# Optimization experiments

Hardware: AMD Instinct MI355X
Metric: run time of the kernel (lower is better)

## Reference

```python
import jax, jax.numpy as jnp
import numpy as np

H_IMG, W_IMG = 160, 160
C1, C2, HEADS, NHOPS = 128, 256, 8, 2
N_NODES = H_IMG * W_IMG


def build_edges(H, W):
    # 3x3 neighborhood (excl. self) + skip edges (i+2,j),(i,j+2); self loops added once
    node = (np.arange(H)[:, None] * W + np.arange(W)[None, :])
    offsets = [(di, dj) for di in (-1, 0, 1) for dj in (-1, 0, 1) if (di, dj) != (0, 0)] + [(2, 0), (0, 2)]
    srcs, dsts = [], []
    for di, dj in offsets:
        i0, i1 = max(0, -di), H - max(0, di)
        j0, j1 = max(0, -dj), W - max(0, dj)
        srcs.append(node[i0:i1, j0:j1].ravel())
        dsts.append(node[i0 + di:i1 + di, j0 + dj:j1 + dj].ravel())
    n = np.arange(H * W)
    srcs.append(n); dsts.append(n)
    return (np.concatenate(srcs).astype(np.int32), np.concatenate(dsts).astype(np.int32))


def setup_inputs() -> dict:
    key = jax.random.key(0)
    ks = jax.random.split(key, 16)
    s = 0.05
    src_np, dst_np = build_edges(H_IMG, W_IMG)
    d = C2 // HEADS
    return {
        "x": jax.random.normal(ks[0], (1, C1, H_IMG, W_IMG), jnp.float32),
        "w_id": jax.random.normal(ks[1], (C2, C1), jnp.float32) * s,
        "w_in": jax.random.normal(ks[2], (C2, C1), jnp.float32) * s,
        "w_gat": jax.random.normal(ks[3], (NHOPS, C2, C2), jnp.float32) * s,
        "a_src": jax.random.normal(ks[4], (NHOPS, HEADS, d), jnp.float32) * s,
        "a_dst": jax.random.normal(ks[5], (NHOPS, HEADS, d), jnp.float32) * s,
        "gat_bias": jax.random.normal(ks[6], (NHOPS, C2), jnp.float32) * s,
        "bn_gamma": jax.random.uniform(ks[7], (NHOPS, C2), jnp.float32, 0.5, 1.5),
        "bn_beta": jax.random.normal(ks[8], (NHOPS, C2), jnp.float32) * s,
        "bn_mean": jax.random.normal(ks[9], (NHOPS, C2), jnp.float32) * s,
        "bn_var": jax.random.uniform(ks[10], (NHOPS, C2), jnp.float32, 0.5, 1.5),
        "w_out": jax.random.normal(ks[11], (C2, C2), jnp.float32) * s,
        "se_w1": jax.random.normal(ks[12], (C2 // 4, C2), jnp.float32) * s,
        "se_b1": jax.random.normal(ks[13], (C2 // 4,), jnp.float32) * s,
        "se_w2": jax.random.normal(ks[14], (C2, C2 // 4), jnp.float32) * s,
        "se_b2": jax.random.normal(ks[15], (C2,), jnp.float32) * s,
        "src": jnp.asarray(src_np),
        "dst": jnp.asarray(dst_np),
    }


def _gat(x, W, a_s, a_d, b, src, dst, N):
    heads, d = a_s.shape
    h = (x @ W.T).reshape(N, heads, d)                      # [N,H,D]
    al_s = jnp.einsum('nhd,hd->nh', h, a_s)                 # [N,H]
    al_d = jnp.einsum('nhd,hd->nh', h, a_d)
    e = jax.nn.leaky_relu(al_s[src] + al_d[dst], 0.2)       # [E,H]
    emax = jax.lax.stop_gradient(jax.ops.segment_max(e, dst, num_segments=N))
    ee = jnp.exp(e - emax[dst])
    denom = jax.ops.segment_sum(ee, dst, num_segments=N)
    alpha = ee / (denom[dst] + 1e-16)                       # segment softmax over incoming edges
    out = jax.ops.segment_sum(h[src] * alpha[..., None], dst, num_segments=N)
    return out.reshape(N, heads * d) + b


def _forward(x, w_id, w_in, w_gat, a_src, a_dst, gat_bias, bn_gamma, bn_beta,
             bn_mean, bn_var, w_out, se_w1, se_b1, se_w2, se_b2, src, dst):
    identity = jnp.einsum('bchw,oc->bohw', x, w_id)
    h = jnp.einsum('bchw,oc->bohw', x, w_in)
    B, C, H, W = h.shape
    N = B * H * W
    xf = h.transpose(0, 2, 3, 1).reshape(N, C)
    for l in range(NHOPS):
        res = xf
        g = _gat(xf, w_gat[l], a_src[l], a_dst[l], gat_bias[l], src, dst, N)
        g = (g - bn_mean[l]) * (bn_gamma[l] * jax.lax.rsqrt(bn_var[l] + 1e-5)) + bn_beta[l]
        xf = jax.nn.relu(g) + res
    y = xf.reshape(B, H, W, C).transpose(0, 3, 1, 2)
    y = jnp.einsum('bchw,oc->bohw', y, w_out)
    # SE block
    w = y.mean(axis=(2, 3))                                 # [B,C]
    w = jax.nn.relu(w @ se_w1.T + se_b1)
    w = jax.nn.sigmoid(w @ se_w2.T + se_b2)
    y = y * w[:, :, None, None]
    return y + identity


def reference(x, w_id, w_in, w_gat, a_src, a_dst, gat_bias, bn_gamma, bn_beta,
              bn_mean, bn_var, w_out, se_w1, se_b1, se_w2, se_b2, src, dst):
    return _forward(x, w_id, w_in, w_gat, a_src, a_dst, gat_bias, bn_gamma, bn_beta,
                    bn_mean, bn_var, w_out, se_w1, se_b1, se_w2, se_b2, src, dst)
```

## Files before the change

kernel.cpp:

```cpp
#include <hip/hip_runtime.h>

#define NN 25600
#define HH 160
#define WW 160
#define C2 256

#define B_WIN   0
#define B_WID   32768
#define B_WGAT  65536
#define B_WOUT  196608
#define B_WEND  262144

#define C_BNA   0
#define C_BNB   512
#define C_ASRC  1024
#define C_ADST  1536
#define C_SEW1  2048
#define C_SEB1  18432
#define C_SEW2  18496
#define C_SEB2  34880
#define C_END   35136

typedef __attribute__((ext_vector_type(8))) short bfrag;
typedef __attribute__((ext_vector_type(4))) float ffrag;
// ... 36 lines not shown
    unsigned short* __restrict__ wb, float* __restrict__ cvt,
    float* __restrict__ means, unsigned short* __restrict__ xT)
{
    __shared__ unsigned short T[64 * 136];
    const bool f32 = probe_f32(xp);
    const int tid = threadIdx.x;
    const int bid = blockIdx.x;
    const int gid = bid * 256 + tid;
    const int stride = gridDim.x * 256;

    if (bid == 0) means[tid] = 0.f;

    for (int i = gid; i < B_WEND; i += stride) {
        const void* s; int o;
        if      (i < B_WID)   { s = pwin;  o = i - B_WIN; }
        else if (i < B_WGAT)  { s = pwid;  o = i - B_WID; }
        else if (i < B_WOUT)  { s = pwgat; o = i - B_WGAT; }
        else                  { s = pwout; o = i - B_WOUT; }
        wb[i] = f32 ? f2b(((const float*)s)[o]) : ((const unsigned short*)s)[o];
    }
    for (int i = gid; i < 512; i += stride) {
        float sc = ldf(pbng, i, f32) * rsqrtf(ldf(pbnv, i, f32) + 1e-5f);
        cvt[C_BNA + i] = sc;
        cvt[C_BNB + i] = (ldf(pgbias, i, f32) - ldf(pbnm, i, f32)) * sc + ldf(pbnb, i, f32);
        cvt[C_ASRC + i] = ldf(pasrc, i, f32);
        cvt[C_ADST + i] = ldf(padst, i, f32);
    }
    for (int i = gid; i < 16384; i += stride) {
        cvt[C_SEW1 + i] = ldf(psew1, i, f32);
        cvt[C_SEW2 + i] = ldf(psew2, i, f32);
    }
    for (int i = gid; i < 64; i += stride)  cvt[C_SEB1 + i] = ldf(pseb1, i, f32);
    for (int i = gid; i < 256; i += stride) cvt[C_SEB2 + i] = ldf(pseb2, i, f32);

    {
        const int n0 = bid * 64;
        const int nl = tid & 63;
#pragma unroll
        for (int i = 0; i < 32; ++i) {
            int c = i * 4 + (tid >> 6);
            long idx = (long)c * NN + n0 + nl;
            T[nl * 136 + c] = f32 ? f2b(((const float*)xp)[idx]) : xp[idx];
        }
        __syncthreads();
#pragma unroll
        for (int i = 0; i < 4; ++i) {
            int n = tid >> 2, c0 = (tid & 3) * 32 + i * 8;
            uint4 v = *(const uint4*)&T[n * 136 + c0];
            *(uint4*)(xT + (long)(n0 + n) * 128 + c0) = v;
        }
    }
}

struct SmemG2 { unsigned short As[128*40], Bi[64*40], Bd[64*40]; };
struct SmemG  { unsigned short As[128*40], Bs[64*40]; };
struct SmemC  { unsigned short Cs[128*72]; };
union  SmemX2 { SmemG2 s; SmemC c; };
union  SmemNN { SmemG s; SmemC c; };

__global__ __launch_bounds__(256) void mfma_gemm_x2_kernel(
    const unsigned short* __restrict__ A16,
    const unsigned short* __restrict__ Wi16,
    const unsigned short* __restrict__ Wd16,
    unsigned short* __restrict__ xf16,
    unsigned short* __restrict__ idb16)
{
    __shared__ SmemX2 sm;
    const int tid = threadIdx.x;
    const int m0 = blockIdx.x * 128, o0 = blockIdx.y * 64;
    const int lane = tid & 63, wv = tid >> 6;
    const int wm = wv >> 1, wn = wv & 1;
    const int lr = lane & 15, quad = lane >> 4;

    ffrag ai[4][2], ad[4][2];
#pragma unroll
    for (int mt = 0; mt < 4; ++mt)
#pragma unroll
        for (int nt = 0; nt < 2; ++nt) { ai[mt][nt] = (ffrag){0,0,0,0}; ad[mt][nt] = (ffrag){0,0,0,0}; }

    for (int k0 = 0; k0 < 128; k0 += 32) {
#pragma unroll
        for (int c = tid; c < 512; c += 256) {
            int row = c >> 2, q = c & 3;
            uint4 v = *(const uint4*)(A16 + (long)(m0 + row) * 128 + k0 + q * 8);
            *(uint4*)&sm.s.As[row * 40 + q * 8] = v;
        }
        {
            int row = tid >> 2, q = tid & 3;
            uint4 vi = *(const uint4*)(Wi16 + (long)(o0 + row) * 128 + k0 + q * 8);
            uint4 vd = *(const uint4*)(Wd16 + (long)(o0 + row) * 128 + k0 + q * 8);
            *(uint4*)&sm.s.Bi[row * 40 + q * 8] = vi;
            *(uint4*)&sm.s.Bd[row * 40 + q * 8] = vd;
        }
        __syncthreads();
        bfrag a[4], bi[2], bd[2];
#pragma unroll
        for (int mt = 0; mt < 4; ++mt)
            a[mt] = *(const bfrag*)&sm.s.As[(wm * 64 + mt * 16 + lr) * 40 + quad * 8];
#pragma unroll
        for (int nt = 0; nt < 2; ++nt) {
            bi[nt] = *(const bfrag*)&sm.s.Bi[(wn * 32 + nt * 16 + lr) * 40 + quad * 8];
            bd[nt] = *(const bfrag*)&sm.s.Bd[(wn * 32 + nt * 16 + lr) * 40 + quad * 8];
        }
#pragma unroll
        for (int mt = 0; mt < 4; ++mt)
#pragma unroll
            for (int nt = 0; nt < 2; ++nt) {
                ai[mt][nt] = __builtin_amdgcn_mfma_f32_16x16x32_bf16(a[mt], bi[nt], ai[mt][nt], 0, 0, 0);
                ad[mt][nt] = __builtin_amdgcn_mfma_f32_16x16x32_bf16(a[mt], bd[nt], ad[mt][nt], 0, 0, 0);
            }
        __syncthreads();
    }
#pragma unroll
    for (int mt = 0; mt < 4; ++mt)
#pragma unroll
        for (int nt = 0; nt < 2; ++nt)
#pragma unroll
            for (int r = 0; r < 4; ++r)
                sm.c.Cs[(wm * 64 + mt * 16 + quad * 4 + r) * 72 + wn * 32 + nt * 16 + lr] = f2b(ai[mt][nt][r]);
    __syncthreads();
#pragma unroll
    for (int it = 0; it < 4; ++it) {
        int e = it * 256 + tid;
        int row = e >> 3, c8 = (e & 7) * 8;
        *(uint4*)(xf16 + (long)(m0 + row) * C2 + o0 + c8) = *(const uint4*)&sm.c.Cs[row * 72 + c8];
    }
    __syncthreads();
#pragma unroll
    for (int mt = 0; mt < 4; ++mt)
#pragma unroll
        for (int nt = 0; nt < 2; ++nt)
#pragma unroll
            for (int r = 0; r < 4; ++r)
                sm.c.Cs[(wm * 64 + mt * 16 + quad * 4 + r) * 72 + wn * 32 + nt * 16 + lr] = f2b(ad[mt][nt][r]);
    __syncthreads();
#pragma unroll
    for (int it = 0; it < 4; ++it) {
        int e = it * 256 + tid;
        int row = e >> 3, c8 = (e & 7) * 8;
        *(uint4*)(idb16 + (long)(m0 + row) * C2 + o0 + c8) = *(const uint4*)&sm.c.Cs[row * 72 + c8];
    }
}

__global__ __launch_bounds__(256) void mfma_gemm_nn_kernel(
    const unsigned short* __restrict__ A16,
    const unsigned short* __restrict__ W16,
    unsigned short* __restrict__ C16,
    const float* __restrict__ asrc, const float* __restrict__ adst,
    float* __restrict__ al_s, float* __restrict__ al_d,
    float* __restrict__ means,
    int mode)
{
    __shared__ SmemNN sm;
    const int tid = threadIdx.x;
    const int m0 = blockIdx.x * 128, o0 = blockIdx.y * 64;
    const int lane = tid & 63, wv = tid >> 6;
    const int wm = wv >> 1, wn = wv & 1;
    const int lr = lane & 15, quad = lane >> 4;

    ffrag acc[4][2];
#pragma unroll
    for (int mt = 0; mt < 4; ++mt)
#pragma unroll
        for (int nt = 0; nt < 2; ++nt) acc[mt][nt] = (ffrag){0,0,0,0};

    for (int k0 = 0; k0 < 256; k0 += 32) {
#pragma unroll
        for (int c = tid; c < 512; c += 256) {
            int row = c >> 2, q = c & 3;
            uint4 v = *(const uint4*)(A16 + (long)(m0 + row) * 256 + k0 + q * 8);
            *(uint4*)&sm.s.As[row * 40 + q * 8] = v;
        }
        {
            int row = tid >> 2, q = tid & 3;
            uint4 v = *(const uint4*)(W16 + (long)(o0 + row) * 256 + k0 + q * 8);
            *(uint4*)&sm.s.Bs[row * 40 + q * 8] = v;
        }
        __syncthreads();
        bfrag a[4], b[2];
#pragma unroll
        for (int mt = 0; mt < 4; ++mt)
            a[mt] = *(const bfrag*)&sm.s.As[(wm * 64 + mt * 16 + lr) * 40 + quad * 8];
#pragma unroll
        for (int nt = 0; nt < 2; ++nt)
            b[nt] = *(const bfrag*)&sm.s.Bs[(wn * 32 + nt * 16 + lr) * 40 + quad * 8];
#pragma unroll
        for (int mt = 0; mt < 4; ++mt)
#pragma unroll
            for (int nt = 0; nt < 2; ++nt)
                acc[mt][nt] = __builtin_amdgcn_mfma_f32_16x16x32_bf16(a[mt], b[nt], acc[mt][nt], 0, 0, 0);
        __syncthreads();
    }
#pragma unroll
    for (int mt = 0; mt < 4; ++mt)
#pragma unroll
        for (int nt = 0; nt < 2; ++nt)
#pragma unroll
            for (int r = 0; r < 4; ++r)
                sm.c.Cs[(wm * 64 + mt * 16 + quad * 4 + r) * 72 + wn * 32 + nt * 16 + lr] = f2b(acc[mt][nt][r]);
    __syncthreads();
#pragma unroll
    for (int it = 0; it < 4; ++it) {
        int e = it * 256 + tid;
        int row = e >> 3, c8 = (e & 7) * 8;
        *(uint4*)(C16 + (long)(m0 + row) * C2 + o0 + c8) = *(const uint4*)&sm.c.Cs[row * 72 + c8];
    }
    if (mode == 1) {
        const int head = blockIdx.y * 2 + wn;
        const float as0 = asrc[head * 32 + lr], as1 = asrc[head * 32 + 16 + lr];
        const float ad0 = adst[head * 32 + lr], ad1 = adst[head * 32 + 16 + lr];
#pragma unroll
        for (int mt = 0; mt < 4; ++mt)
#pragma unroll
            for (int r = 0; r < 4; ++r) {
                float ps = acc[mt][0][r] * as0 + acc[mt][1][r] * as1;
                float pd = acc[mt][0][r] * ad0 + acc[mt][1][r] * ad1;
#pragma unroll
                for (int sh = 1; sh < 16; sh <<= 1) {
                    ps += __shfl_xor(ps, sh);
                    pd += __shfl_xor(pd, sh);
                }
                if (lr == 0) {
                    int m = m0 + wm * 64 + mt * 16 + quad * 4 + r;
                    al_s[m * 8 + head] = ps;
                    al_d[m * 8 + head] = pd;
                }
            }
    } else if (mode == 2) {
#pragma unroll
        for (int nt = 0; nt < 2; ++nt) {
            float p = 0.f;
#pragma unroll
            for (int mt = 0; mt < 4; ++mt)
#pragma unroll
                for (int r = 0; r < 4; ++r) p += acc[mt][nt][r];
            p += __shfl_xor(p, 16);
            p += __shfl_xor(p, 32);
            if (quad == 0) atomicAdd(&means[o0 + wn * 32 + nt * 16 + lr], p);
        }
    }
}

__global__ __launch_bounds__(256) void aggregate_kernel(
    const unsigned short* __restrict__ h16,
    const float* __restrict__ al_s,
    const float* __restrict__ al_d,
    const float* __restrict__ bnA,
    const float* __restrict__ bnB,
    unsigned short* __restrict__ xf16)
{
    const int SI[11] = { 1, 1, 1, 0, 0, -1, -1, -1, -2,  0, 0};
    const int SJ[11] = { 1, 0,-1, 1,-1,  1,  0, -1,  0, -2, 0};
    __shared__ float es[8][11][8];
    __shared__ float alpha[8][11][8];

    const int t = threadIdx.x;
    const int ln = t >> 5;
    const int l = t & 31;
    const int n = blockIdx.x * 8 + ln;
    const int i = n / WW, j = n % WW;

    for (int idx = t; idx < 704; idx += 256) {
        int lln = idx / 88, rem = idx - lln * 88;
        int k = rem >> 3, hh = rem & 7;
        int nn2 = blockIdx.x * 8 + lln;
        int ii = nn2 / WW, jj = nn2 - ii * WW;
        int si = ii + SI[k], sj = jj + SJ[k];
        bool okk = (si >= 0) & (si < HH) & (sj >= 0) & (sj < WW);
        es[lln][k][hh] = okk ? al_s[(si * WW + sj) * 8 + hh] : -1e30f;
    }
    __syncthreads();

    if (l < 8) {
        const int hd = l;
        const float ald = al_d[n * 8 + hd];
        float e[11];
        float mx = -1e30f;
#pragma unroll
        for (int k = 0; k < 11; ++k) {
            float v = es[ln][k][hd] + ald;
            v = v > 0.f ? v : 0.2f * v;
            e[k] = v;
            mx = fmaxf(mx, v);
        }
        float denom = 0.f;
#pragma unroll
        for (int k = 0; k < 11; ++k) {
            float p = __expf(e[k] - mx);
            e[k] = p;
            denom += p;
        }
        const float inv = 1.f / (denom + 1e-16f);
#pragma unroll
        for (int k = 0; k < 11; ++k) alpha[ln][k][hd] = e[k] * inv;
    }
    __syncthreads();

    const int c8 = l * 8;
    const int hd = l >> 2;
    int srcn[11];
#pragma unroll
    for (int k = 0; k < 11; ++k) {
        int si = i + SI[k], sj = j + SJ[k];
        bool ok = (si >= 0) & (si < HH) & (sj >= 0) & (sj < WW);
        srcn[k] = ok ? si * WW + sj : n;
    }
    float a0=0.f,a1=0.f,a2=0.f,a3=0.f,a4=0.f,a5=0.f,a6=0.f,a7=0.f;
#pragma unroll
    for (int k = 0; k < 11; ++k) {
        float al = alpha[ln][k][hd];
        uint4 hv = *(const uint4*)(h16 + (long)srcn[k] * C2 + c8);
        a0 += al * lo16f(hv.x); a1 += al * hi16f(hv.x);
        a2 += al * lo16f(hv.y); a3 += al * hi16f(hv.y);
        a4 += al * lo16f(hv.z); a5 += al * hi16f(hv.z);
        a6 += al * lo16f(hv.w); a7 += al * hi16f(hv.w);
    }
    float acc8[8] = {a0,a1,a2,a3,a4,a5,a6,a7};
    uint4 rv = *(const uint4*)(xf16 + (long)n * C2 + c8);
    float res[8] = {lo16f(rv.x),hi16f(rv.x),lo16f(rv.y),hi16f(rv.y),
                    lo16f(rv.z),hi16f(rv.z),lo16f(rv.w),hi16f(rv.w)};
    float out[8];
#pragma unroll
    for (int q = 0; q < 8; ++q) {
        int c = c8 + q;
        float g = acc8[q] * bnA[c] + bnB[c];
        out[q] = fmaxf(g, 0.f) + res[q];
    }
    ushort4 o16a, o16b;
    o16a.x = f2b(out[0]); o16a.y = f2b(out[1]); o16a.z = f2b(out[2]); o16a.w = f2b(out[3]);
    o16b.x = f2b(out[4]); o16b.y = f2b(out[5]); o16b.z = f2b(out[6]); o16b.w = f2b(out[7]);
    *(ushort4*)(xf16 + (long)n * C2 + c8)     = o16a;
    *(ushort4*)(xf16 + (long)n * C2 + c8 + 4) = o16b;
}

__global__ __launch_bounds__(256) void final_kernel(
    const unsigned short* __restrict__ x_probe,
    const unsigned short* __restrict__ y16,
    const unsigned short* __restrict__ idb16,
    const float* __restrict__ means,
    const float* __restrict__ cvt,
    void* __restrict__ outp)
{
    __shared__ float T[64][65];
    __shared__ float mv[256];
    __shared__ float hv[64];
    __shared__ float sv[64];
    const bool f32o = probe_f32(x_probe);
    const int t = threadIdx.x;
    const int n0 = blockIdx.x * 64, c0 = blockIdx.y * 64;

    mv[t] = means[t] * (1.0f / 25600.0f);
    __syncthreads();
    if (t < 64) {
        const float* w1 = cvt + C_SEW1 + t * 256;
        float s = cvt[C_SEB1 + t];
        for (int cc = 0; cc < 256; cc += 4) {
            float4 wv = *(const float4*)(w1 + cc);
            s += wv.x * mv[cc] + wv.y * mv[cc+1] + wv.z * mv[cc+2] + wv.w * mv[cc+3];
        }
        hv[t] = fmaxf(s, 0.f);
    }
    __syncthreads();
    if (t < 64) {
        const int c = c0 + t;
        const float* w2 = cvt + C_SEW2 + c * 64;
        float s = cvt[C_SEB2 + c];
        for (int k = 0; k < 64; k += 4) {
            float4 wv = *(const float4*)(w2 + k);
            s += wv.x * hv[k] + wv.y * hv[k+1] + wv.z * hv[k+2] + wv.w * hv[k+3];
        }
        sv[t] = 1.0f / (1.0f + __expf(-s));
    }
    __syncthreads();
#pragma unroll
    for (int it = 0; it < 16; ++it) {
        int e = t + it * 256;
        int nn = e >> 6, cc = e & 63;
        long idx = (long)(n0 + nn) * C2 + c0 + cc;
        T[cc][nn] = b2f(y16[idx]) * sv[cc] + b2f(idb16[idx]);
    }
    __syncthreads();
#pragma unroll
    for (int it = 0; it < 16; ++it) {
        int e = t + it * 256;
        int cc = e >> 6, nn = e & 63;
        long idx = (long)(c0 + cc) * NN + n0 + nn;
        float v = T[cc][nn];
        if (f32o) ((float*)outp)[idx] = v;
        else      ((unsigned short*)outp)[idx] = f2b(v);
    }
}

extern "C" void kernel_launch(void* const* d_in, const int* in_sizes, int n_in,
                              void* d_out, int out_size, void* d_ws, size_t ws_size,
                              hipStream_t stream) {
    float* ws = (float*)d_ws;
    float* cvt   = ws;
    float* means = ws + 35200;
    float* als   = means + 256;
    float* ald   = als + 204800;
    unsigned short* wb16  = (unsigned short*)(ald + 204800);
    unsigned short* xT16  = wb16 + B_WEND;
    unsigned short* xf16  = xT16 + NN * 128;
    unsigned short* h16   = xf16 + NN * 256;
    unsigned short* idb16 = h16 + NN * 256;

    const unsigned short* xp = (const unsigned short*)d_in[0];

    dim3 b256(256);
    dim3 gmfma(NN / 128, C2 / 64);
    dim3 gfin(NN / 64, C2 / 64);

    prep_kernel<<<400, b256, 0, stream>>>(
        xp, d_in[2], d_in[1], d_in[3], d_in[11],
        d_in[4], d_in[5], d_in[6], d_in[7], d_in[8], d_in[9], d_in[10],
        d_in[12], d_in[13], d_in[14], d_in[15],
        wb16, cvt, means, xT16);

    mfma_gemm_x2_kernel<<<gmfma, b256, 0, stream>>>(
        xT16, wb16 + B_WIN, wb16 + B_WID, xf16, idb16);

    for (int l = 0; l < 2; ++l) {
        mfma_gemm_nn_kernel<<<gmfma, b256, 0, stream>>>(
            xf16, wb16 + B_WGAT + l * 65536, h16,
            cvt + C_ASRC + l * 256, cvt + C_ADST + l * 256, als, ald, nullptr, 1);
        aggregate_kernel<<<NN / 8, b256, 0, stream>>>(h16, als, ald,
            cvt + C_BNA + l * 256, cvt + C_BNB + l * 256, xf16);
    }

    mfma_gemm_nn_kernel<<<gmfma, b256, 0, stream>>>(
        xf16, wb16 + B_WOUT, h16, nullptr, nullptr, nullptr, nullptr, means, 2);
    final_kernel<<<gfin, b256, 0, stream>>>(xp, h16, idb16, means, cvt, d_out);
}
```

Before: 239.7 us.

## Fuse GAT aggregation into following GEMM with full-width 512-thread tiles

Result: slower. 294.1 us (+22.7%).

```diff
diff --git a/kernel.cpp b/kernel.cpp
--- a/kernel.cpp
+++ b/kernel.cpp
@@ -113,10 +113,12 @@
 }
 
 struct SmemG2 { unsigned short As[128*40], Bi[64*40], Bd[64*40]; };
-struct SmemG  { unsigned short As[128*40], Bs[64*40]; };
 struct SmemC  { unsigned short Cs[128*72]; };
 union  SmemX2 { SmemG2 s; SmemC c; };
-union  SmemNN { SmemG s; SmemC c; };
+
+struct SmemFG { unsigned short As[128*40], Bs[256*40]; };
+struct SmemFA { float es[128][11][8]; };
+union  SmemF  { SmemFG g; SmemFA a; SmemC c; };
 
 __global__ __launch_bounds__(256) void mfma_gemm_x2_kernel(
     const unsigned short* __restrict__ A16,
@@ -202,93 +204,157 @@
     }
 }
 
-__global__ __launch_bounds__(256) void mfma_gemm_nn_kernel(
-    const unsigned short* __restrict__ A16,
+__global__ __launch_bounds__(512) void fused_gat_kernel(
+    unsigned short* __restrict__ xf16,
+    const unsigned short* __restrict__ h_in,
+    const float* __restrict__ als_in, const float* __restrict__ ald_in,
+    const float* __restrict__ bnA, const float* __restrict__ bnB,
     const unsigned short* __restrict__ W16,
-    unsigned short* __restrict__ C16,
+    unsigned short* __restrict__ Cout,
     const float* __restrict__ asrc, const float* __restrict__ adst,
-    float* __restrict__ al_s, float* __restrict__ al_d,
-    float* __restrict__ means,
-    int mode)
+    float* __restrict__ als_out, float* __restrict__ ald_out,
+    float* __restrict__ means, int mode)
 {
-    __shared__ SmemNN sm;
+    __shared__ SmemF sm;
     const int tid = threadIdx.x;
-    const int m0 = blockIdx.x * 128, o0 = blockIdx.y * 64;
+    const int m0 = blockIdx.x * 128;
     const int lane = tid & 63, wv = tid >> 6;
-    const int wm = wv >> 1, wn = wv & 1;
+    const int wm = wv >> 2, wn = wv & 3;
     const int lr = lane & 15, quad = lane >> 4;
 
-    ffrag acc[4][2];
+    const int SI[11] = { 1, 1, 1, 0, 0, -1, -1, -1, -2,  0, 0};
+    const int SJ[11] = { 1, 0,-1, 1,-1,  1,  0, -1,  0, -2, 0};
+
+    if (h_in) {
+        for (int idx = tid; idx < 11264; idx += 512) {
+            int ln = idx / 88, rem = idx - ln * 88;
+            int k = rem >> 3, hh = rem & 7;
+            int n2 = m0 + ln, ii = n2 / WW, jj = n2 - ii * WW;
+            int si = ii + SI[k], sj = jj + SJ[k];
+            bool ok = (si >= 0) & (si < HH) & (sj >= 0) & (sj < WW);
+            sm.a.es[ln][k][hh] = ok ? als_in[(si * WW + sj) * 8 + hh] : -1e30f;
+        }
+        __syncthreads();
+        for (int p = tid; p < 1024; p += 512) {
+            int ln = p >> 3, hd = p & 7;
+            float ad = ald_in[(m0 + ln) * 8 + hd];
+            float e[11];
+            float mx = -1e30f;
+#pragma unroll
+            for (int k = 0; k < 11; ++k) {
+                float v = sm.a.es[ln][k][hd] + ad;
+                v = v > 0.f ? v : 0.2f * v;
+                e[k] = v;
+                mx = fmaxf(mx, v);
+            }
+            float den = 0.f;
+#pragma unroll
+            for (int k = 0; k < 11; ++k) { float q = __expf(e[k] - mx); e[k] = q; den += q; }
+            float inv = 1.f / (den + 1e-16f);
+#pragma unroll
+            for (int k = 0; k < 11; ++k) sm.a.es[ln][k][hd] = e[k] * inv;
+        }
+        __syncthreads();
+        {
+            const int cj = tid & 31, c8 = cj * 8, hd = cj >> 2;
+            for (int q = 0; q < 8; ++q) {
+                int ln = q * 16 + (tid >> 5);
+                int n = m0 + ln, i = n / WW, j = n - i * WW;
+                float acc8[8] = {0,0,0,0,0,0,0,0};
+#pragma unroll
+                for (int k = 0; k < 11; ++k) {
+                    int si = i + SI[k], sj = j + SJ[k];
+                    bool ok = (si >= 0) & (si < HH) & (sj >= 0) & (sj < WW);
+                    int srcn = ok ? si * WW + sj : n;
+                    float al = sm.a.es[ln][k][hd];
+                    uint4 hv = *(const uint4*)(h_in + (long)srcn * C2 + c8);
+                    acc8[0] += al * lo16f(hv.x); acc8[1] += al * hi16f(hv.x);
+                    acc8[2] += al * lo16f(hv.y); acc8[3] += al * hi16f(hv.y);
+                    acc8[4] += al * lo16f(hv.z); acc8[5] += al * hi16f(hv.z);
+                    acc8[6] += al * lo16f(hv.w); acc8[7] += al * hi16f(hv.w);
+                }
+                uint4 rv = *(const uint4*)(xf16 + (long)n * C2 + c8);
+                float res[8] = {lo16f(rv.x),hi16f(rv.x),lo16f(rv.y),hi16f(rv.y),
+                                lo16f(rv.z),hi16f(rv.z),lo16f(rv.w),hi16f(rv.w)};
+                unsigned short o[8];
+#pragma unroll
+                for (int q2 = 0; q2 < 8; ++q2) {
+                    int c = c8 + q2;
+                    float g = acc8[q2] * bnA[c] + bnB[c];
+                    o[q2] = f2b(fmaxf(g, 0.f) + res[q2]);
+                }
+                uint4 ov;
+                ov.x = (unsigned int)o[0] | ((unsigned int)o[1] << 16);
+                ov.y = (unsigned int)o[2] | ((unsigned int)o[3] << 16);
+                ov.z = (unsigned int)o[4] | ((unsigned int)o[5] << 16);
+                ov.w = (unsigned int)o[6] | ((unsigned int)o[7] << 16);
+                *(uint4*)(xf16 + (long)n * C2 + c8) = ov;
+            }
+        }
+        __syncthreads();
+    }
+
+    ffrag acc[4][4];
 #pragma unroll
     for (int mt = 0; mt < 4; ++mt)
 #pragma unroll
-        for (int nt = 0; nt < 2; ++nt) acc[mt][nt] = (ffrag){0,0,0,0};
+        for (int nt = 0; nt < 4; ++nt) acc[mt][nt] = (ffrag){0,0,0,0};
 
     for (int k0 = 0; k0 < 256; k0 += 32) {
-#pragma unroll
-        for (int c = tid; c < 512; c += 256) {
-            int row = c >> 2, q = c & 3;
-            uint4 v = *(const uint4*)(A16 + (long)(m0 + row) * 256 + k0 + q * 8);
-            *(uint4*)&sm.s.As[row * 40 + q * 8] = v;
-        }
         {
             int row = tid >> 2, q = tid & 3;
-            uint4 v = *(const uint4*)(W16 + (long)(o0 + row) * 256 + k0 + q * 8);
-            *(uint4*)&sm.s.Bs[row * 40 + q * 8] = v;
-        }
-        __syncthreads();
-        bfrag a[4], b[2];
+            uint4 v = *(const uint4*)(xf16 + (long)(m0 + row) * C2 + k0 + q * 8);
+            *(uint4*)&sm.g.As[row * 40 + q * 8] = v;
+        }
+#pragma unroll
+        for (int c = tid; c < 1024; c += 512) {
+            int row = c >> 2, q = c & 3;
+            uint4 v = *(const uint4*)(W16 + (long)row * C2 + k0 + q * 8);
+            *(uint4*)&sm.g.Bs[row * 40 + q * 8] = v;
+        }
+        __syncthreads();
+        bfrag a[4], b[4];
 #pragma unroll
         for (int mt = 0; mt < 4; ++mt)
-            a[mt] = *(const bfrag*)&sm.s.As[(wm * 64 + mt * 16 + lr) * 40 + quad * 8];
-#pragma unroll
-        for (int nt = 0; nt < 2; ++nt)
-            b[nt] = *(const bfrag*)&sm.s.Bs[(wn * 32 + nt * 16 + lr) * 40 + quad * 8];
+            a[mt] = *(const bfrag*)&sm.g.As[(wm * 64 + mt * 16 + lr) * 40 + quad * 8];
+#pragma unroll
+        for (int nt = 0; nt < 4; ++nt)
+            b[nt] = *(const bfrag*)&sm.g.Bs[(wn * 64 + nt * 16 + lr) * 40 + quad * 8];
 #pragma unroll
         for (int mt = 0; mt < 4; ++mt)
 #pragma unroll
-            for (int nt = 0; nt < 2; ++nt)
+            for (int nt = 0; nt < 4; ++nt)
                 acc[mt][nt] = __builtin_amdgcn_mfma_f32_16x16x32_bf16(a[mt], b[nt], acc[mt][nt], 0, 0, 0);
         __syncthreads();
     }
-#pragma unroll
-    for (int mt = 0; mt < 4; ++mt)
-#pragma unroll
-        for (int nt = 0; nt < 2; ++nt)
-#pragma unroll
-            for (int r = 0; r < 4; ++r)
-                sm.c.Cs[(wm * 64 + mt * 16 + quad * 4 + r) * 72 + wn * 32 + nt * 16 + lr] = f2b(acc[mt][nt][r]);
-    __syncthreads();
-#pragma unroll
-    for (int it = 0; it < 4; ++it) {
-        int e = it * 256 + tid;
-        int row = e >> 3, c8 = (e & 7) * 8;
-        *(uint4*)(C16 + (long)(m0 + row) * C2 + o0 + c8) = *(const uint4*)&sm.c.Cs[row * 72 + c8];
-    }
+
     if (mode == 1) {
-        const int head = blockIdx.y * 2 + wn;
-        const float as0 = asrc[head * 32 + lr], as1 = asrc[head * 32 + 16 + lr];
-        const float ad0 = adst[head * 32 + lr], ad1 = adst[head * 32 + 16 + lr];
-#pragma unroll
-        for (int mt = 0; mt < 4; ++mt)
-#pragma unroll
-            for (int r = 0; r < 4; ++r) {
-                float ps = acc[mt][0][r] * as0 + acc[mt][1][r] * as1;
-                float pd = acc[mt][0][r] * ad0 + acc[mt][1][r] * ad1;
-#pragma unroll
-                for (int sh = 1; sh < 16; sh <<= 1) {
-                    ps += __shfl_xor(ps, sh);
-                    pd += __shfl_xor(pd, sh);
+#pragma unroll
+        for (int hh = 0; hh < 2; ++hh) {
+            const int head = wn * 2 + hh;
+            const float as_lo = asrc[head * 32 + lr], as_hi = asrc[head * 32 + 16 + lr];
+            const float ad_lo = adst[head * 32 + lr], ad_hi = adst[head * 32 + 16 + lr];
+#pragma unroll
+            for (int mt = 0; mt < 4; ++mt)
+#pragma unroll
+                for (int r = 0; r < 4; ++r) {
+                    float ps = acc[mt][2*hh][r] * as_lo + acc[mt][2*hh+1][r] * as_hi;
+                    float pd = acc[mt][2*hh][r] * ad_lo + acc[mt][2*hh+1][r] * ad_hi;
+#pragma unroll
+                    for (int sh = 1; sh < 16; sh <<= 1) {
+                        ps += __shfl_xor(ps, sh);
+                        pd += __shfl_xor(pd, sh);
+                    }
+                    if (lr == 0) {
+                        int m = m0 + wm * 64 + mt * 16 + quad * 4 + r;
+                        als_out[m * 8 + head] = ps;
+                        ald_out[m * 8 + head] = pd;
+                    }
                 }
-                if (lr == 0) {
-                    int m = m0 + wm * 64 + mt * 16 + quad * 4 + r;
-                    al_s[m * 8 + head] = ps;
-                    al_d[m * 8 + head] = pd;
-                }
-            }
+        }
     } else if (mode == 2) {
 #pragma unroll
-        for (int nt = 0; nt < 2; ++nt) {
+        for (int nt = 0; nt < 4; ++nt) {
             float p = 0.f;
 #pragma unroll
             for (int mt = 0; mt < 4; ++mt)
@@ -296,101 +362,30 @@
                 for (int r = 0; r < 4; ++r) p += acc[mt][nt][r];
             p += __shfl_xor(p, 16);
             p += __shfl_xor(p, 32);
-            if (quad == 0) atomicAdd(&means[o0 + wn * 32 + nt * 16 + lr], p);
-        }
-    }
-}
-
-__global__ __launch_bounds__(256) void aggregate_kernel(
-    const unsigned short* __restrict__ h16,
-    const float* __restrict__ al_s,
-    const float* __restrict__ al_d,
-    const float* __restrict__ bnA,
-    const float* __restrict__ bnB,
-    unsigned short* __restrict__ xf16)
-{
-    const int SI[11] = { 1, 1, 1, 0, 0, -1, -1, -1, -2,  0, 0};
-    const int SJ[11] = { 1, 0,-1, 1,-1,  1,  0, -1,  0, -2, 0};
-    __shared__ float es[8][11][8];
-    __shared__ float alpha[8][11][8];
-
-    const int t = threadIdx.x;
-    const int ln = t >> 5;
-    const int l = t & 31;
-    const int n = blockIdx.x * 8 + ln;
-    const int i = n / WW, j = n % WW;
-
-    for (int idx = t; idx < 704; idx += 256) {
-        int lln = idx / 88, rem = idx - lln * 88;
-        int k = rem >> 3, hh = rem & 7;
-        int nn2 = blockIdx.x * 8 + lln;
-        int ii = nn2 / WW, jj = nn2 - ii * WW;
-        int si = ii + SI[k], sj = jj + SJ[k];
-        bool okk = (si >= 0) & (si < HH) & (sj >= 0) & (sj < WW);
-        es[lln][k][hh] = okk ? al_s[(si * WW + sj) * 8 + hh] : -1e30f;
-    }
-    __syncthreads();
-
-    if (l < 8) {
-        const int hd = l;
-        const float ald = al_d[n * 8 + hd];
-        float e[11];
-        float mx = -1e30f;
-#pragma unroll
-        for (int k = 0; k < 11; ++k) {
-            float v = es[ln][k][hd] + ald;
-            v = v > 0.f ? v : 0.2f * v;
-            e[k] = v;
-            mx = fmaxf(mx, v);
-        }
-        float denom = 0.f;
-#pragma unroll
-        for (int k = 0; k < 11; ++k) {
-            float p = __expf(e[k] - mx);
-            e[k] = p;
-            denom += p;
-        }
-        const float inv = 1.f / (denom + 1e-16f);
-#pragma unroll
-        for (int k = 0; k < 11; ++k) alpha[ln][k][hd] = e[k] * inv;
-    }
-    __syncthreads();
-
-    const int c8 = l * 8;
-    const int hd = l >> 2;
-    int srcn[11];
-#pragma unroll
-    for (int k = 0; k < 11; ++k) {
-        int si = i + SI[k], sj = j + SJ[k];
-        bool ok = (si >= 0) & (si < HH) & (sj >= 0) & (sj < WW);
-        srcn[k] = ok ? si * WW + sj : n;
-    }
-    float a0=0.f,a1=0.f,a2=0.f,a3=0.f,a4=0.f,a5=0.f,a6=0.f,a7=0.f;
-#pragma unroll
-    for (int k = 0; k < 11; ++k) {
-        float al = alpha[ln][k][hd];
-        uint4 hv = *(const uint4*)(h16 + (long)srcn[k] * C2 + c8);
-        a0 += al * lo16f(hv.x); a1 += al * hi16f(hv.x);
-        a2 += al * lo16f(hv.y); a3 += al * hi16f(hv.y);
-        a4 += al * lo16f(hv.z); a5 += al * hi16f(hv.z);
-        a6 += al * lo16f(hv.w); a7 += al * hi16f(hv.w);
-    }
-    float acc8[8] = {a0,a1,a2,a3,a4,a5,a6,a7};
-    uint4 rv = *(const uint4*)(xf16 + (long)n * C2 + c8);
-    float res[8] = {lo16f(rv.x),hi16f(rv.x),lo16f(rv.y),hi16f(rv.y),
-                    lo16f(rv.z),hi16f(rv.z),lo16f(rv.w),hi16f(rv.w)};
-    float out[8];
-#pragma unroll
-    for (int q = 0; q < 8; ++q) {
-        int c = c8 + q;
-        float g = acc8[q] * bnA[c] + bnB[c];
-        out[q] = fmaxf(g, 0.f) + res[q];
-    }
-    ushort4 o16a, o16b;
-    o16a.x = f2b(out[0]); o16a.y = f2b(out[1]); o16a.z = f2b(out[2]); o16a.w = f2b(out[3]);
-    o16b.x = f2b(out[4]); o16b.y = f2b(out[5]); o16b.z = f2b(out[6]); o16b.w = f2b(out[7]);
-    *(ushort4*)(xf16 + (long)n * C2 + c8)     = o16a;
-    *(ushort4*)(xf16 + (long)n * C2 + c8 + 4) = o16b;
+            if (quad == 0) atomicAdd(&means[wn * 64 + nt * 16 + lr], p);
+        }
+    }
+
+#pragma unroll
+    for (int pc = 0; pc < 4; ++pc) {
+        if (wn == pc) {
+#pragma unroll
+            for (int mt = 0; mt < 4; ++mt)
+#pragma unroll
+                for (int nt = 0; nt < 4; ++nt)
+#pragma unroll
+                    for (int r = 0; r < 4; ++r)
+                        sm.c.Cs[(wm * 64 + mt * 16 + quad * 4 + r) * 72 + nt * 16 + lr] = f2b(acc[mt][nt][r]);
+        }
+        __syncthreads();
+#pragma unroll
+        for (int it = 0; it < 2; ++it) {
+            int e = it * 512 + tid;
+            int row = e >> 3, c8 = (e & 7) * 8;
+            *(uint4*)(Cout + (long)(m0 + row) * C2 + pc * 64 + c8) = *(const uint4*)&sm.c.Cs[row * 72 + c8];
+        }
+        __syncthreads();
+    }
 }
 
 __global__ __launch_bounds__(256) void final_kernel(
@@ -457,18 +452,23 @@
     float* ws = (float*)d_ws;
     float* cvt   = ws;
     float* means = ws + 35200;
-    float* als   = means + 256;
-    float* ald   = als + 204800;
-    unsigned short* wb16  = (unsigned short*)(ald + 204800);
+    float* als1  = means + 256;
+    float* ald1  = als1 + 204800;
+    float* als2  = ald1 + 204800;
+    float* ald2  = als2 + 204800;
+    unsigned short* wb16  = (unsigned short*)(ald2 + 204800);
     unsigned short* xT16  = wb16 + B_WEND;
     unsigned short* xf16  = xT16 + NN * 128;
-    unsigned short* h16   = xf16 + NN * 256;
-    unsigned short* idb16 = h16 + NN * 256;
+    unsigned short* h1    = xf16 + NN * 256;
+    unsigned short* h2    = h1 + NN * 256;
+    unsigned short* idb16 = h2 + NN * 256;
 
     const unsigned short* xp = (const unsigned short*)d_in[0];
 
     dim3 b256(256);
+    dim3 b512(512);
     dim3 gmfma(NN / 128, C2 / 64);
+    dim3 gfus(NN / 128);
     dim3 gfin(NN / 64, C2 / 64);
 
     prep_kernel<<<400, b256, 0, stream>>>(
@@ -480,15 +480,20 @@
     mfma_gemm_x2_kernel<<<gmfma, b256, 0, stream>>>(
         xT16, wb16 + B_WIN, wb16 + B_WID, xf16, idb16);
 
-    for (int l = 0; l < 2; ++l) {
-        mfma_gemm_nn_kernel<<<gmfma, b256, 0, stream>>>(
-            xf16, wb16 + B_WGAT + l * 65536, h16,
-            cvt + C_ASRC + l * 256, cvt + C_ADST + l * 256, als, ald, nullptr, 1);
-        aggregate_kernel<<<NN / 8, b256, 0, stream>>>(h16, als, ald,
-            cvt + C_BNA + l * 256, cvt + C_BNB + l * 256, xf16);
-    }
-
-    mfma_gemm_nn_kernel<<<gmfma, b256, 0, stream>>>(
-        xf16, wb16 + B_WOUT, h16, nullptr, nullptr, nullptr, nullptr, means, 2);
-    final_kernel<<<gfin, b256, 0, stream>>>(xp, h16, idb16, means, cvt, d_out);
-}
+    fused_gat_kernel<<<gfus, b512, 0, stream>>>(
+        xf16, nullptr, nullptr, nullptr, nullptr, nullptr,
+        wb16 + B_WGAT, h1,
+        cvt + C_ASRC, cvt + C_ADST, als1, ald1, nullptr, 1);
+
+    fused_gat_kernel<<<gfus, b512, 0, stream>>>(
+        xf16, h1, als1, ald1, cvt + C_BNA, cvt + C_BNB,
+        wb16 + B_WGAT + 65536, h2,
+        cvt + C_ASRC + 256, cvt + C_ADST + 256, als2, ald2, nullptr, 1);
+
+    fused_gat_kernel<<<gfus, b512, 0, stream>>>(
+        xf16, h2, als2, ald2, cvt + C_BNA + 256, cvt + C_BNB + 256,
+        wb16 + B_WOUT, h1,
+        nullptr, nullptr, nullptr, nullptr, means, 2);
+
+    final_kernel<<<gfin, b256, 0, stream>>>(xp, h1, idb16, means, cvt, d_out);
+}
```

## Fuse output GEMM with SE and residual epilogue; compute SE mean via linearity

Applied to the files above, without the earlier changes.

Measured after the change: 331.2 us. +38.2%, slower.

```diff
diff --git a/kernel.cpp b/kernel.cpp
--- a/kernel.cpp
+++ b/kernel.cpp
@@ -112,11 +112,14 @@
     }
 }
 
-struct SmemG2 { unsigned short As[128*40], Bi[64*40], Bd[64*40]; };
-struct SmemG  { unsigned short As[128*40], Bs[64*40]; };
-struct SmemC  { unsigned short Cs[128*72]; };
-union  SmemX2 { SmemG2 s; SmemC c; };
-union  SmemNN { SmemG s; SmemC c; };
+struct SmemC64 { unsigned short Cs[64 * 72]; };
+struct SmemNN2 { unsigned short As[64 * 72], Bs[64 * 72]; };
+union  SmemN   { SmemNN2 g; SmemC64 c; };
+struct SmemX2G { unsigned short As[64*72], Bi[64*72], Bd[64*72]; };
+union  SmemX   { SmemX2G g; SmemC64 c; };
+struct SmemFGm { unsigned short As[64*72], Bs[256*72]; };
+struct SmemT   { float T[64 * 73]; };
+union  SmemFin { SmemFGm g; SmemT t; };
 
 __global__ __launch_bounds__(256) void mfma_gemm_x2_kernel(
     const unsigned short* __restrict__ A16,
@@ -125,152 +128,131 @@
     unsigned short* __restrict__ xf16,
     unsigned short* __restrict__ idb16)
 {
-    __shared__ SmemX2 sm;
+    __shared__ SmemX sm;
     const int tid = threadIdx.x;
-    const int m0 = blockIdx.x * 128, o0 = blockIdx.y * 64;
+    const int m0 = blockIdx.x * 64, o0 = blockIdx.y * 64;
     const int lane = tid & 63, wv = tid >> 6;
     const int wm = wv >> 1, wn = wv & 1;
     const int lr = lane & 15, quad = lane >> 4;
 
-    ffrag ai[4][2], ad[4][2];
-#pragma unroll
-    for (int mt = 0; mt < 4; ++mt)
+    ffrag ai[2][2], ad[2][2];
+#pragma unroll
+    for (int mt = 0; mt < 2; ++mt)
 #pragma unroll
         for (int nt = 0; nt < 2; ++nt) { ai[mt][nt] = (ffrag){0,0,0,0}; ad[mt][nt] = (ffrag){0,0,0,0}; }
 
-    for (int k0 = 0; k0 < 128; k0 += 32) {
-#pragma unroll
-        for (int c = tid; c < 512; c += 256) {
-            int row = c >> 2, q = c & 3;
-            uint4 v = *(const uint4*)(A16 + (long)(m0 + row) * 128 + k0 + q * 8);
-            *(uint4*)&sm.s.As[row * 40 + q * 8] = v;
-        }
-        {
-            int row = tid >> 2, q = tid & 3;
-            uint4 vi = *(const uint4*)(Wi16 + (long)(o0 + row) * 128 + k0 + q * 8);
-            uint4 vd = *(const uint4*)(Wd16 + (long)(o0 + row) * 128 + k0 + q * 8);
-            *(uint4*)&sm.s.Bi[row * 40 + q * 8] = vi;
-            *(uint4*)&sm.s.Bd[row * 40 + q * 8] = vd;
-        }
-        __syncthreads();
-        bfrag a[4], bi[2], bd[2];
-#pragma unroll
-        for (int mt = 0; mt < 4; ++mt)
-            a[mt] = *(const bfrag*)&sm.s.As[(wm * 64 + mt * 16 + lr) * 40 + quad * 8];
-#pragma unroll
-        for (int nt = 0; nt < 2; ++nt) {
-            bi[nt] = *(const bfrag*)&sm.s.Bi[(wn * 32 + nt * 16 + lr) * 40 + quad * 8];
-            bd[nt] = *(const bfrag*)&sm.s.Bd[(wn * 32 + nt * 16 + lr) * 40 + quad * 8];
-        }
-#pragma unroll
-        for (int mt = 0; mt < 4; ++mt)
+    for (int k0 = 0; k0 < 128; k0 += 64) {
+#pragma unroll
+        for (int e = tid; e < 512; e += 256) {
+            int row = e >> 3, q = e & 7;
+            *(uint4*)&sm.g.As[row * 72 + q * 8] = *(const uint4*)(A16 + (long)(m0 + row) * 128 + k0 + q * 8);
+            *(uint4*)&sm.g.Bi[row * 72 + q * 8] = *(const uint4*)(Wi16 + (long)(o0 + row) * 128 + k0 + q * 8);
+            *(uint4*)&sm.g.Bd[row * 72 + q * 8] = *(const uint4*)(Wd16 + (long)(o0 + row) * 128 + k0 + q * 8);
+        }
+        __syncthreads();
+#pragma unroll
+        for (int ks = 0; ks < 2; ++ks) {
+            bfrag a[2], bi[2], bd[2];
+#pragma unroll
+            for (int mt = 0; mt < 2; ++mt)
+                a[mt] = *(const bfrag*)&sm.g.As[(wm * 32 + mt * 16 + lr) * 72 + ks * 32 + quad * 8];
 #pragma unroll
             for (int nt = 0; nt < 2; ++nt) {
-                ai[mt][nt] = __builtin_amdgcn_mfma_f32_16x16x32_bf16(a[mt], bi[nt], ai[mt][nt], 0, 0, 0);
-                ad[mt][nt] = __builtin_amdgcn_mfma_f32_16x16x32_bf16(a[mt], bd[nt], ad[mt][nt], 0, 0, 0);
+                bi[nt] = *(const bfrag*)&sm.g.Bi[(wn * 32 + nt * 16 + lr) * 72 + ks * 32 + quad * 8];
+                bd[nt] = *(const bfrag*)&sm.g.Bd[(wn * 32 + nt * 16 + lr) * 72 + ks * 32 + quad * 8];
             }
-        __syncthreads();
-    }
-#pragma unroll
-    for (int mt = 0; mt < 4; ++mt)
+#pragma unroll
+            for (int mt = 0; mt < 2; ++mt)
+#pragma unroll
+                for (int nt = 0; nt < 2; ++nt) {
+                    ai[mt][nt] = __builtin_amdgcn_mfma_f32_16x16x32_bf16(a[mt], bi[nt], ai[mt][nt], 0, 0, 0);
+                    ad[mt][nt] = __builtin_amdgcn_mfma_f32_16x16x32_bf16(a[mt], bd[nt], ad[mt][nt], 0, 0, 0);
+                }
+        }
+        __syncthreads();
+    }
+#pragma unroll
+    for (int mt = 0; mt < 2; ++mt)
 #pragma unroll
         for (int nt = 0; nt < 2; ++nt)
 #pragma unroll
             for (int r = 0; r < 4; ++r)
-                sm.c.Cs[(wm * 64 + mt * 16 + quad * 4 + r) * 72 + wn * 32 + nt * 16 + lr] = f2b(ai[mt][nt][r]);
-    __syncthreads();
-#pragma unroll
-    for (int it = 0; it < 4; ++it) {
+                sm.c.Cs[(wm * 32 + mt * 16 + quad * 4 + r) * 72 + wn * 32 + nt * 16 + lr] = f2b(ai[mt][nt][r]);
+    __syncthreads();
+#pragma unroll
+    for (int it = 0; it < 2; ++it) {
         int e = it * 256 + tid;
         int row = e >> 3, c8 = (e & 7) * 8;
         *(uint4*)(xf16 + (long)(m0 + row) * C2 + o0 + c8) = *(const uint4*)&sm.c.Cs[row * 72 + c8];
     }
     __syncthreads();
 #pragma unroll
-    for (int mt = 0; mt < 4; ++mt)
+    for (int mt = 0; mt < 2; ++mt)
 #pragma unroll
         for (int nt = 0; nt < 2; ++nt)
 #pragma unroll
             for (int r = 0; r < 4; ++r)
-                sm.c.Cs[(wm * 64 + mt * 16 + quad * 4 + r) * 72 + wn * 32 + nt * 16 + lr] = f2b(ad[mt][nt][r]);
-    __syncthreads();
-#pragma unroll
-    for (int it = 0; it < 4; ++it) {
+                sm.c.Cs[(wm * 32 + mt * 16 + quad * 4 + r) * 72 + wn * 32 + nt * 16 + lr] = f2b(ad[mt][nt][r]);
+    __syncthreads();
+#pragma unroll
+    for (int it = 0; it < 2; ++it) {
         int e = it * 256 + tid;
         int row = e >> 3, c8 = (e & 7) * 8;
         *(uint4*)(idb16 + (long)(m0 + row) * C2 + o0 + c8) = *(const uint4*)&sm.c.Cs[row * 72 + c8];
     }
 }
 
-__global__ __launch_bounds__(256) void mfma_gemm_nn_kernel(
+__global__ __launch_bounds__(256) void gat_gemm_kernel(
     const unsigned short* __restrict__ A16,
     const unsigned short* __restrict__ W16,
-    unsigned short* __restrict__ C16,
+    unsigned short* __restrict__ Cout,
     const float* __restrict__ asrc, const float* __restrict__ adst,
-    float* __restrict__ al_s, float* __restrict__ al_d,
-    float* __restrict__ means,
-    int mode)
+    float* __restrict__ als_out, float* __restrict__ ald_out)
 {
-    __shared__ SmemNN sm;
+    __shared__ SmemN sm;
     const int tid = threadIdx.x;
-    const int m0 = blockIdx.x * 128, o0 = blockIdx.y * 64;
+    const int m0 = blockIdx.x * 64, o0 = blockIdx.y * 64;
     const int lane = tid & 63, wv = tid >> 6;
     const int wm = wv >> 1, wn = wv & 1;
     const int lr = lane & 15, quad = lane >> 4;
 
-    ffrag acc[4][2];
-#pragma unroll
-    for (int mt = 0; mt < 4; ++mt)
+    ffrag acc[2][2];
+#pragma unroll
+    for (int mt = 0; mt < 2; ++mt)
 #pragma unroll
         for (int nt = 0; nt < 2; ++nt) acc[mt][nt] = (ffrag){0,0,0,0};
 
-    for (int k0 = 0; k0 < 256; k0 += 32) {
-#pragma unroll
-        for (int c = tid; c < 512; c += 256) {
-            int row = c >> 2, q = c & 3;
-            uint4 v = *(const uint4*)(A16 + (long)(m0 + row) * 256 + k0 + q * 8);
-            *(uint4*)&sm.s.As[row * 40 + q * 8] = v;
-        }
-        {
-            int row = tid >> 2, q = tid & 3;
-            uint4 v = *(const uint4*)(W16 + (long)(o0 + row) * 256 + k0 + q * 8);
-            *(uint4*)&sm.s.Bs[row * 40 + q * 8] = v;
-        }
-        __syncthreads();
-        bfrag a[4], b[2];
-#pragma unroll
-        for (int mt = 0; mt < 4; ++mt)
-            a[mt] = *(const bfrag*)&sm.s.As[(wm * 64 + mt * 16 + lr) * 40 + quad * 8];
-#pragma unroll
-        for (int nt = 0; nt < 2; ++nt)
-            b[nt] = *(const bfrag*)&sm.s.Bs[(wn * 32 + nt * 16 + lr) * 40 + quad * 8];
-#pragma unroll
-        for (int mt = 0; mt < 4; ++mt)
+    for (int k0 = 0; k0 < 256; k0 += 64) {
+#pragma unroll
+        for (int e = tid; e < 512; e += 256) {
+            int row = e >> 3, q = e & 7;
+            *(uint4*)&sm.g.As[row * 72 + q * 8] = *(const uint4*)(A16 + (long)(m0 + row) * C2 + k0 + q * 8);
+            *(uint4*)&sm.g.Bs[row * 72 + q * 8] = *(const uint4*)(W16 + (long)(o0 + row) * C2 + k0 + q * 8);
+        }
+        __syncthreads();
+#pragma unroll
+        for (int ks = 0; ks < 2; ++ks) {
+            bfrag a[2], b[2];
+#pragma unroll
+            for (int mt = 0; mt < 2; ++mt)
+                a[mt] = *(const bfrag*)&sm.g.As[(wm * 32 + mt * 16 + lr) * 72 + ks * 32 + quad * 8];
 #pragma unroll
             for (int nt = 0; nt < 2; ++nt)
-                acc[mt][nt] = __builtin_amdgcn_mfma_f32_16x16x32_bf16(a[mt], b[nt], acc[mt][nt], 0, 0, 0);
-        __syncthreads();
-    }
-#pragma unroll
-    for (int mt = 0; mt < 4; ++mt)
-#pragma unroll
-        for (int nt = 0; nt < 2; ++nt)
-#pragma unroll
-            for (int r = 0; r < 4; ++r)
-                sm.c.Cs[(wm * 64 + mt * 16 + quad * 4 + r) * 72 + wn * 32 + nt * 16 + lr] = f2b(acc[mt][nt][r]);
-    __syncthreads();
-#pragma unroll
-    for (int it = 0; it < 4; ++it) {
-        int e = it * 256 + tid;
-        int row = e >> 3, c8 = (e & 7) * 8;
-        *(uint4*)(C16 + (long)(m0 + row) * C2 + o0 + c8) = *(const uint4*)&sm.c.Cs[row * 72 + c8];
-    }
-    if (mode == 1) {
+                b[nt] = *(const bfrag*)&sm.g.Bs[(wn * 32 + nt * 16 + lr) * 72 + ks * 32 + quad * 8];
+#pragma unroll
+            for (int mt = 0; mt < 2; ++mt)
+#pragma unroll
+                for (int nt = 0; nt < 2; ++nt)
+                    acc[mt][nt] = __builtin_amdgcn_mfma_f32_16x16x32_bf16(a[mt], b[nt], acc[mt][nt], 0, 0, 0);
+        }
+        __syncthreads();
+    }
+    {
         const int head = blockIdx.y * 2 + wn;
         const float as0 = asrc[head * 32 + lr], as1 = asrc[head * 32 + 16 + lr];
         const float ad0 = adst[head * 32 + lr], ad1 = adst[head * 32 + 16 + lr];
 #pragma unroll
-        for (int mt = 0; mt < 4; ++mt)
+        for (int mt = 0; mt < 2; ++mt)
 #pragma unroll
             for (int r = 0; r < 4; ++r) {
                 float ps = acc[mt][0][r] * as0 + acc[mt][1][r] * as1;
@@ -281,23 +263,25 @@
                     pd += __shfl_xor(pd, sh);
                 }
                 if (lr == 0) {
-                    int m = m0 + wm * 64 + mt * 16 + quad * 4 + r;
-                    al_s[m * 8 + head] = ps;
-                    al_d[m * 8 + head] = pd;
+                    int m = m0 + wm * 32 + mt * 16 + quad * 4 + r;
+                    als_out[m * 8 + head] = ps;
+                    ald_out[m * 8 + head] = pd;
                 }
             }
-    } else if (mode == 2) {
-#pragma unroll
-        for (int nt = 0; nt < 2; ++nt) {
-            float p = 0.f;
-#pragma unroll
-            for (int mt = 0; mt < 4; ++mt)
-#pragma unroll
-                for (int r = 0; r < 4; ++r) p += acc[mt][nt][r];
-            p += __shfl_xor(p, 16);
-            p += __shfl_xor(p, 32);
-            if (quad == 0) atomicAdd(&means[o0 + wn * 32 + nt * 16 + lr], p);
-        }
+    }
+#pragma unroll
+    for (int mt = 0; mt < 2; ++mt)
+#pragma unroll
+        for (int nt = 0; nt < 2; ++nt)
+#pragma unroll
+            for (int r = 0; r < 4; ++r)
+                sm.c.Cs[(wm * 32 + mt * 16 + quad * 4 + r) * 72 + wn * 32 + nt * 16 + lr] = f2b(acc[mt][nt][r]);
+    __syncthreads();
+#pragma unroll
+    for (int it = 0; it < 2; ++it) {
+        int e = it * 256 + tid;
+        int row = e >> 3, c8 = (e & 7) * 8;
+        *(uint4*)(Cout + (long)(m0 + row) * C2 + o0 + c8) = *(const uint4*)&sm.c.Cs[row * 72 + c8];
     }
 }
 
@@ -393,61 +377,149 @@
     *(ushort4*)(xf16 + (long)n * C2 + c8 + 4) = o16b;
 }
 
-__global__ __launch_bounds__(256) void final_kernel(
+__global__ __launch_bounds__(256) void colsum_kernel(
+    const unsigned short* __restrict__ xf16, float* __restrict__ means)
+{
+    const int t = threadIdx.x;
+    const int rg = t >> 5;
+    const int c8 = (t & 31) * 8;
+    const long r0 = blockIdx.x * 256;
+    float s[8] = {0,0,0,0,0,0,0,0};
+    for (int r = rg; r < 256; r += 8) {
+        uint4 v = *(const uint4*)(xf16 + (r0 + r) * C2 + c8);
+        s[0] += lo16f(v.x); s[1] += hi16f(v.x);
+        s[2] += lo16f(v.y); s[3] += hi16f(v.y);
+        s[4] += lo16f(v.z); s[5] += hi16f(v.z);
+        s[6] += lo16f(v.w); s[7] += hi16f(v.w);
+    }
+#pragma unroll
+    for (int q = 0; q < 8; ++q) s[q] += __shfl_xor(s[q], 32);
+    if ((t & 63) < 32) {
+#pragma unroll
+        for (int q = 0; q < 8; ++q) atomicAdd(&means[c8 + q], s[q]);
+    }
+}
+
+__global__ __launch_bounds__(256) void final_gemm_kernel(
     const unsigned short* __restrict__ x_probe,
-    const unsigned short* __restrict__ y16,
+    const unsigned short* __restrict__ A16,
+    const unsigned short* __restrict__ W16,
     const unsigned short* __restrict__ idb16,
     const float* __restrict__ means,
     const float* __restrict__ cvt,
     void* __restrict__ outp)
 {
-    __shared__ float T[64][65];
-    __shared__ float mv[256];
-    __shared__ float hv[64];
-    __shared__ float sv[64];
+    __shared__ SmemFin sm;
+    __shared__ float cs[256], mv[256], hv[64], sv[256];
     const bool f32o = probe_f32(x_probe);
-    const int t = threadIdx.x;
-    const int n0 = blockIdx.x * 64, c0 = blockIdx.y * 64;
-
-    mv[t] = means[t] * (1.0f / 25600.0f);
-    __syncthreads();
-    if (t < 64) {
-        const float* w1 = cvt + C_SEW1 + t * 256;
-        float s = cvt[C_SEB1 + t];
+    const int tid = threadIdx.x;
+    const int m0 = blockIdx.x * 64;
+    const int lane = tid & 63, wv = tid >> 6;
+    const int wm = wv >> 1, wn = wv & 1;
+    const int lr = lane & 15, quad = lane >> 4;
+
+    ffrag acc[2][8];
+#pragma unroll
+    for (int mt = 0; mt < 2; ++mt)
+#pragma unroll
+        for (int nt = 0; nt < 8; ++nt) acc[mt][nt] = (ffrag){0,0,0,0};
+
+    for (int k0 = 0; k0 < 256; k0 += 64) {
+#pragma unroll
+        for (int e = tid; e < 512; e += 256) {
+            int row = e >> 3, q = e & 7;
+            *(uint4*)&sm.g.As[row * 72 + q * 8] = *(const uint4*)(A16 + (long)(m0 + row) * C2 + k0 + q * 8);
+        }
+#pragma unroll
+        for (int e = tid; e < 2048; e += 256) {
+            int row = e >> 3, q = e & 7;
+            *(uint4*)&sm.g.Bs[row * 72 + q * 8] = *(const uint4*)(W16 + (long)row * C2 + k0 + q * 8);
+        }
+        __syncthreads();
+#pragma unroll
+        for (int ks = 0; ks < 2; ++ks) {
+            bfrag a[2], b[8];
+#pragma unroll
+            for (int mt = 0; mt < 2; ++mt)
+                a[mt] = *(const bfrag*)&sm.g.As[(wm * 32 + mt * 16 + lr) * 72 + ks * 32 + quad * 8];
+#pragma unroll
+            for (int nt = 0; nt < 8; ++nt)
+                b[nt] = *(const bfrag*)&sm.g.Bs[(wn * 128 + nt * 16 + lr) * 72 + ks * 32 + quad * 8];
+#pragma unroll
+            for (int mt = 0; mt < 2; ++mt)
+#pragma unroll
+                for (int nt = 0; nt < 8; ++nt)
+                    acc[mt][nt] = __builtin_amdgcn_mfma_f32_16x16x32_bf16(a[mt], b[nt], acc[mt][nt], 0, 0, 0);
+        }
+        __syncthreads();
+    }
+
+    cs[tid] = means[tid];
+    __syncthreads();
+    {
+        float s = 0.f;
+        const unsigned short* wr = W16 + (long)tid * C2;
+#pragma unroll 4
+        for (int k = 0; k < 256; k += 8) {
+            uint4 w = *(const uint4*)(wr + k);
+            s += cs[k]   * lo16f(w.x) + cs[k+1] * hi16f(w.x)
+               + cs[k+2] * lo16f(w.y) + cs[k+3] * hi16f(w.y)
+               + cs[k+4] * lo16f(w.z) + cs[k+5] * hi16f(w.z)
+               + cs[k+6] * lo16f(w.w) + cs[k+7] * hi16f(w.w);
+        }
+        mv[tid] = s * (1.0f / 25600.0f);
+    }
+    __syncthreads();
+    if (tid < 64) {
+        const float* w1 = cvt + C_SEW1 + tid * 256;
+        float s = cvt[C_SEB1 + tid];
         for (int cc = 0; cc < 256; cc += 4) {
-            float4 wv = *(const float4*)(w1 + cc);
-            s += wv.x * mv[cc] + wv.y * mv[cc+1] + wv.z * mv[cc+2] + wv.w * mv[cc+3];
-        }
-        hv[t] = fmaxf(s, 0.f);
-    }
-    __syncthreads();
-    if (t < 64) {
-        const int c = c0 + t;
-        const float* w2 = cvt + C_SEW2 + c * 64;
-        float s = cvt[C_SEB2 + c];
+            float4 w = *(const float4*)(w1 + cc);
+            s += w.x * mv[cc] + w.y * mv[cc+1] + w.z * mv[cc+2] + w.w * mv[cc+3];
+        }
+        hv[tid] = fmaxf(s, 0.f);
+    }
+    __syncthreads();
+    {
+        const float* w2 = cvt + C_SEW2 + tid * 64;
+        float s = cvt[C_SEB2 + tid];
         for (int k = 0; k < 64; k += 4) {
-            float4 wv = *(const float4*)(w2 + k);
-            s += wv.x * hv[k] + wv.y * hv[k+1] + wv.z * hv[k+2] + wv.w * hv[k+3];
-        }
-        sv[t] = 1.0f / (1.0f + __expf(-s));
-    }
-    __syncthreads();
-#pragma unroll
-    for (int it = 0; it < 16; ++it) {
-        int e = t + it * 256;
-        int nn = e >> 6, cc = e & 63;
-        long idx = (long)(n0 + nn) * C2 + c0 + cc;
-        T[cc][nn] = b2f(y16[idx]) * sv[cc] + b2f(idb16[idx]);
-    }
-    __syncthreads();
-#pragma unroll
-    for (int it = 0; it < 16; ++it) {
-        int e = t + it * 256;
-        int cc = e >> 6, nn = e & 63;
-        long idx = (long)(c0 + cc) * NN + n0 + nn;
-        float v = T[cc][nn];
-        if (f32o) ((float*)outp)[idx] = v;
-        else      ((unsigned short*)outp)[idx] = f2b(v);
+            float4 w = *(const float4*)(w2 + k);
+            s += w.x * hv[k] + w.y * hv[k+1] + w.z * hv[k+2] + w.w * hv[k+3];
+        }
+        sv[tid] = 1.0f / (1.0f + __expf(-s));
+    }
+    __syncthreads();
+
+#pragma unroll
+    for (int pc = 0; pc < 4; ++pc) {
+        if (wn == (pc >> 1)) {
+#pragma unroll
+            for (int mt = 0; mt < 2; ++mt)
+#pragma unroll
+                for (int nt4 = 0; nt4 < 4; ++nt4) {
+                    int nt = (pc & 1) * 4 + nt4;
+                    int col = wn * 128 + nt * 16 + lr;
+                    float s = sv[col];
+#pragma unroll
+                    for (int r = 0; r < 4; ++r) {
+                        int row = wm * 32 + mt * 16 + quad * 4 + r;
+                        float v = acc[mt][nt][r] * s + b2f(idb16[(long)(m0 + row) * C2 + col]);
+                        sm.t.T[(nt4 * 16 + lr) * 73 + row] = v;
+                    }
+                }
+        }
+        __syncthreads();
+#pragma unroll
+        for (int it = 0; it < 16; ++it) {
+            int e = it * 256 + tid;
+            int cc = e >> 6, nn = e & 63;
+            long idx = (long)(pc * 64 + cc) * NN + m0 + nn;
+            float v = sm.t.T[cc * 73 + nn];
+            if (f32o) ((float*)outp)[idx] = v;
+            else      ((unsigned short*)outp)[idx] = f2b(v);
+        }
+        __syncthreads();
     }
 }
 
@@ -468,8 +540,8 @@
     const unsigned short* xp = (const unsigned short*)d_in[0];
 
     dim3 b256(256);
-    dim3 gmfma(NN / 128, C2 / 64);
-    dim3 gfin(NN / 64, C2 / 64);
+    dim3 gmfma(NN / 64, C2 / 64);
+    dim3 gfin(NN / 64);
 
     prep_kernel<<<400, b256, 0, stream>>>(
         xp, d_in[2], d_in[1], d_in[3], d_in[11],
@@ -481,14 +553,15 @@
         xT16, wb16 + B_WIN, wb16 + B_WID, xf16, idb16);
 
     for (int l = 0; l < 2; ++l) {
-        mfma_gemm_nn_kernel<<<gmfma, b256, 0, stream>>>(
+        gat_gemm_kernel<<<gmfma, b256, 0, stream>>>(
             xf16, wb16 + B_WGAT + l * 65536, h16,
-            cvt + C_ASRC + l * 256, cvt + C_ADST + l * 256, als, ald, nullptr, 1);
+            cvt + C_ASRC + l * 256, cvt + C_ADST + l * 256, als, ald);
         aggregate_kernel<<<NN / 8, b256, 0, stream>>>(h16, als, ald,
             cvt + C_BNA + l * 256, cvt + C_BNB + l * 256, xf16);
     }
 
-    mfma_gemm_nn_kernel<<<gmfma, b256, 0, stream>>>(
-        xf16, wb16 + B_WOUT, h16, nullptr, nullptr, nullptr, nullptr, means, 2);
-    final_kernel<<<gfin, b256, 0, stream>>>(xp, h16, idb16, means, cvt, d_out);
-}
+    colsum_kernel<<<100, b256, 0, stream>>>(xf16, means);
+
+    final_gemm_kernel<<<gfin, b256, 0, stream>>>(
+        xp, xf16, wb16 + B_WOUT, idb16, means, cvt, d_out);
+}
```
